# Performance work log

Hardware: AMD Instinct MI355X
Metric: run time of the kernel (lower is better)

Reference implementation:

```python
import jax, jax.numpy as jnp
import numpy as np

B, C, S, N, V = 8, 16, 512, 512, 128
EPS = 1e-5

def setup_inputs() -> dict:
    key = jax.random.key(0)
    ks = jax.random.split(key, 9)
    def u(k, shape, scale):
        return jax.random.uniform(k, shape, jnp.float32, -scale, scale)
    attn_scale = 12 * np.sqrt(3.0 / (S * N * V))      # custom attn_init for query / key.left / value2
    xav_vs = np.sqrt(6.0 / (V + S))                    # xavier_uniform for (C, V, S) or (C, S, V)
    xav_nv = np.sqrt(6.0 / (N + V))                    # xavier_uniform for (C, N, V)
    return {
        "x": jax.random.normal(ks[0], (B, C, S, N), jnp.float32),
        "wq": u(ks[1], (C, N, V), attn_scale),          # query weight (other_features=S)
        "k_left": u(ks[2], (C, V, S), attn_scale),      # key left (attn_init)
        "k_right": u(ks[3], (C, N, V), xav_nv),         # key right (xavier)
        "v1_left": u(ks[4], (C, V, S), xav_vs),         # value1 left (xavier, attn_init=False)
        "v1_right": u(ks[5], (C, N, V), attn_scale),    # value1 right (attn_init scale)
        "v2_w": u(ks[6], (C, V, S), attn_scale),        # value2 weight (other_features=N)
        "gamma": jnp.ones((C,), jnp.float32),
        "beta": jnp.zeros((C,), jnp.float32),
    }

def batch_scaler(y, gamma, beta):
    # normalize over dims (0, 2, 3); per-channel affine
    mean = jnp.mean(y, axis=(0, 2, 3), keepdims=True)
    var = jnp.mean(jnp.square(y - mean), axis=(0, 2, 3), keepdims=True)
    yhat = (y - mean) * jax.lax.rsqrt(var + EPS)
    return yhat * gamma[None, :, None, None] + beta[None, :, None, None]

def reference(x, wq, k_left, k_right, v1_left, v1_right, v2_w, gamma, beta):
    # x: [B,C,S,N]
    q = jnp.matmul(x, wq)                               # [B,C,S,V]
    k = jnp.matmul(jnp.matmul(k_left, x), k_right)       # (C,V,S)@x -> [B,C,V,N] @ (C,N,V) -> [B,C,V,V]
    attn = jax.nn.softmax(jnp.einsum('bcsv,bcwv->bcsw', q, k), axis=-1)  # q @ k^T, softmax last dim
    v1 = jnp.matmul(jnp.matmul(v1_left, x), v1_right)    # [B,C,V,V]
    v2 = jnp.matmul(v2_w, x)                             # [B,C,V,N]
    v = jnp.matmul(v1, v2)                               # [B,C,V,N]
    y = x + jnp.matmul(attn, v)                          # [B,C,S,N]
    return batch_scaler(y, gamma, beta)
```

## Files before the change

### kernel.cpp

```cpp
#include <hip/hip_runtime.h>
#include <math.h>


typedef short  bf16x8 __attribute__((ext_vector_type(8)));
typedef short  short8 __attribute__((ext_vector_type(8)));
typedef float  f32x4  __attribute__((ext_vector_type(4)));

__device__ __forceinline__ unsigned short f2bf(float f) {
    union { float f; unsigned u; } v; v.f = f;
    return (unsigned short)((v.u + 0x7FFF + ((v.u >> 16) & 1)) >> 16);
}
__device__ __forceinline__ float bf2f(unsigned short u) {
    union { unsigned u; float f; } v; v.u = (unsigned)u << 16; return v.f;
}

__device__ __forceinline__ void gload16(const void* g, void* l)
{
    __builtin_amdgcn_global_load_lds(
        (const __attribute__((address_space(1))) void*)g,
        (__attribute__((address_space(3))) void*)l, 16, 0, 0);
}

constexpr size_t OB_XB   = 0;
constexpr size_t OB_XT   = OB_XB  + 67108864;
constexpr size_t OB_KLB  = OB_XT  + 67108864;
constexpr size_t OB_V1LB = OB_KLB + 2097152;
constexpr size_t OB_V2WB = OB_V1LB+ 2097152;
constexpr size_t OB_WQT  = OB_V2WB+ 2097152;
constexpr size_t OB_KRT  = OB_WQT + 2097152;
constexpr size_t OB_V1RT = OB_KRT + 2097152;
constexpr size_t OB_BUF  = OB_V1RT+ 2097152;
constexpr size_t OB_V2T  = OB_BUF + 33554432;
constexpr size_t OB_KM   = OB_V2T + 16777216;
constexpr size_t OB_V1M  = OB_KM  + 4194304;
constexpr size_t OB_ATT  = OB_V1M + 4194304;
constexpr size_t OB_VT   = OB_ATT + 16777216;
constexpr size_t OB_ST   = OB_VT  + 16777216;

template<int NSTEPS, int MF, int NF>
__device__ __forceinline__ void mmcore(const char* __restrict__ Ab, int ldaB,
                                       const char* __restrict__ Bb, int ldbB,
                                       f32x4 (&acc)[MF][NF],
                                       char* __restrict__ smA, char* __restrict__ smB,
                                       int wm, int wn)
{
    const int tid = threadIdx.x;
    const int w = tid >> 6, l = tid & 63, g = l >> 4, lr = l & 15;
    const int rl = l >> 3, ch = l & 7;

#pragma unroll 1
    for (int t = 0; t < NSTEPS; ++t) {
#pragma unroll
        for (int j = 0; j < 4; ++j) {
            const int row = w * 32 + j * 8 + rl;
            gload16(Ab + (size_t)row * ldaB + t * 128 + ((ch ^ (row & 7)) * 16),
                    smA + (w * 32 + j * 8) * 128);
        }
#pragma unroll
        for (int j = 0; j < 4; ++j) {
            const int row = w * 32 + j * 8 + rl;
            gload16(Bb + (size_t)row * ldbB + t * 128 + ((ch ^ (row & 7)) * 16),
                    smB + (w * 32 + j * 8) * 128);
        }
        __syncthreads();
#pragma unroll
        for (int ks = 0; ks < 2; ++ks) {
            bf16x8 av[MF], bv[NF];
            const int cc = ks * 4 + g;
#pragma unroll
            for (int i = 0; i < MF; ++i) { int rw = wm + i * 16 + lr;
                av[i] = *(const bf16x8*)(smA + rw * 128 + ((cc ^ (rw & 7)) * 16)); }
#pragma unroll
            for (int j = 0; j < NF; ++j) { int rw = wn + j * 16 + lr;
                bv[j] = *(const bf16x8*)(smB + rw * 128 + ((cc ^ (rw & 7)) * 16)); }
#pragma unroll
            for (int i = 0; i < MF; ++i)
#pragma unroll
                for (int j = 0; j < NF; ++j)
                    acc[i][j] = __builtin_amdgcn_mfma_f32_16x16x32_bf16(av[i], bv[j], acc[i][j], 0, 0, 0);
        }
        __syncthreads();
    }
}

__device__ __forceinline__ void epi_write_rm(const f32x4 (&acc)[4][4], char* sm)
{
    const int tid = threadIdx.x, w = tid >> 6, l = tid & 63, g = l >> 4, lr = l & 15;
    const int wm = (w >> 1) * 64, wn = (w & 1) * 64;
#pragma unroll
    for (int i = 0; i < 4; ++i)
#pragma unroll
        for (int j = 0; j < 4; ++j) {
            const int row = wm + i * 16 + g * 4, col = wn + j * 16 + lr;
#pragma unroll
            for (int r = 0; r < 4; ++r)
                *(unsigned short*)(sm + (row + r) * 272 + col * 2) = f2bf(acc[i][j][r]);
        }
}

__device__ __forceinline__ void epi_write_tr(const f32x4 (&acc)[4][4], char* sm)
{
    const int tid = threadIdx.x, w = tid >> 6, l = tid & 63, g = l >> 4, lr = l & 15;
    const int wm = (w >> 1) * 64, wn = (w & 1) * 64;
#pragma unroll
    for (int i = 0; i < 4; ++i)
#pragma unroll
        for (int j = 0; j < 4; ++j) {
            const int rv = wm + i * 16 + g * 4, cn = wn + j * 16 + lr;
            ushort4 pk = make_ushort4(f2bf(acc[i][j][0]), f2bf(acc[i][j][1]),
                                      f2bf(acc[i][j][2]), f2bf(acc[i][j][3]));
            *(ushort4*)(sm + cn * 272 + rv * 2) = pk;
        }
}

__device__ __forceinline__ void epi_flush(const char* sm, unsigned short* gout, int ldg)
{
    const int tid = threadIdx.x;
    const int r0 = tid >> 4, q = tid & 15;
#pragma unroll
    for (int rep = 0; rep < 8; ++rep) {
        const int row = rep * 16 + r0;
        *(short8*)((short*)gout + (size_t)row * ldg + q * 8) =
            *(const short8*)(sm + row * 272 + q * 16);
    }
    __syncthreads();
}

__global__ __launch_bounds__(256) void k_prep(const float* __restrict__ kl,
                                              const float* __restrict__ v1l,
                                              const float* __restrict__ v2w,
                                              const float* __restrict__ wq,
                                              const float* __restrict__ kr,
                                              const float* __restrict__ v1r,
                                              unsigned short* __restrict__ klb,
                                              unsigned short* __restrict__ v1lb,
                                              unsigned short* __restrict__ v2wb,
                                              unsigned short* __restrict__ wqt,
                                              unsigned short* __restrict__ krt,
                                              unsigned short* __restrict__ v1rt,
                                              float* __restrict__ stats)
{
    __shared__ float tl[64][65];
    const int id = blockIdx.x, tid = threadIdx.x;
    if (id == 0 && tid < 64) stats[tid] = 0.f;
    if (id < 192) {
        const int sel = id >> 6, blk = id & 63;
        const float* src = sel == 0 ? kl : sel == 1 ? v1l : v2w;
        unsigned short* dst = sel == 0 ? klb : sel == 1 ? v1lb : v2wb;
#pragma unroll
        for (int r = 0; r < 4; ++r) {
            const int i = blk * 1024 + r * 256 + tid;
            float4 v = ((const float4*)src)[i];
            ((ushort4*)dst)[i] = make_ushort4(f2bf(v.x), f2bf(v.y), f2bf(v.z), f2bf(v.w));
        }
        return;
    }
    const int id2 = id - 192;
    const int p = id2 >> 4, rem = id2 & 15, by = rem >> 1, bx = rem & 1;
    const int widx = p >> 4, c = p & 15;
    const float* s = (widx == 0 ? wq : widx == 1 ? kr : v1r) + (size_t)c * 65536;
    unsigned short* d = (widx == 0 ? wqt : widx == 1 ? krt : v1rt) + (size_t)c * 65536;
    const int r0 = by * 64, c0 = bx * 64;
    const int rr = tid >> 4, cc = (tid & 15) * 4;
#pragma unroll
    for (int rep = 0; rep < 4; ++rep) {
        int row = rep * 16 + rr;
        float4 v = *(const float4*)(s + (size_t)(r0 + row) * 128 + c0 + cc);
        tl[cc + 0][row] = v.x; tl[cc + 1][row] = v.y; tl[cc + 2][row] = v.z; tl[cc + 3][row] = v.w;
    }
    __syncthreads();
#pragma unroll
    for (int rep = 0; rep < 4; ++rep) {
        int crow = rep * 16 + rr;
        *(ushort4*)(d + (size_t)(c0 + crow) * 512 + r0 + cc) =
            make_ushort4(f2bf(tl[crow][cc]), f2bf(tl[crow][cc + 1]),
                         f2bf(tl[crow][cc + 2]), f2bf(tl[crow][cc + 3]));
    }
}

__global__ __launch_bounds__(256) void ktransx(const float* __restrict__ x,
                                               unsigned short* __restrict__ xb,
                                               unsigned short* __restrict__ xt)
{
    __shared__ float tl[64][65];
    const int bc = blockIdx.z;
    const int r0 = blockIdx.y * 64, c0 = blockIdx.x * 64;
    const float* src = x + (size_t)bc * 262144;
    const int tid = threadIdx.x, rr = tid >> 4, cc = (tid & 15) * 4;
#pragma unroll
    for (int rep = 0; rep < 4; ++rep) {
        int row = rep * 16 + rr;
        float4 v = *(const float4*)(src + (size_t)(r0 + row) * 512 + c0 + cc);
        *(ushort4*)(xb + (size_t)bc * 262144 + (size_t)(r0 + row) * 512 + c0 + cc) =
            make_ushort4(f2bf(v.x), f2bf(v.y), f2bf(v.z), f2bf(v.w));
        tl[cc + 0][row] = v.x; tl[cc + 1][row] = v.y; tl[cc + 2][row] = v.z; tl[cc + 3][row] = v.w;
    }
    __syncthreads();
#pragma unroll
    for (int rep = 0; rep < 4; ++rep) {
        int crow = rep * 16 + rr;
        *(ushort4*)(xt + (size_t)bc * 262144 + (size_t)(c0 + crow) * 512 + r0 + cc) =
            make_ushort4(f2bf(tl[crow][cc]), f2bf(tl[crow][cc + 1]),
                         f2bf(tl[crow][cc + 2]), f2bf(tl[crow][cc + 3]));
    }
}

__global__ __launch_bounds__(256, 2) void k_wx(const unsigned short* __restrict__ klb,
                                               const unsigned short* __restrict__ v1lb,
                                               const unsigned short* __restrict__ v2wb,
                                               const unsigned short* __restrict__ xt,
                                               unsigned short* __restrict__ bufb,
                                               unsigned short* __restrict__ v2t)
{
    __shared__ char smem[34816];
    char* smA = smem; char* smB = smem + 16384;
    const int mt = blockIdx.x >> 2, n0 = blockIdx.x & 3, bc = blockIdx.y, c = bc & 15;
    const unsigned short* W = mt == 0 ? klb : mt == 1 ? v1lb : v2wb;
    const char* Bb = (const char*)(xt + (size_t)bc * 262144 + (size_t)n0 * 65536);
    const int w = threadIdx.x >> 6;
    f32x4 acc[4][4] = {};
    mmcore<8, 4, 4>((const char*)(W + (size_t)c * 65536), 1024, Bb, 1024, acc, smA, smB,
                    (w >> 1) * 64, (w & 1) * 64);
    if (mt < 2) {
        epi_write_rm(acc, smem);
        __syncthreads();
        epi_flush(smem, bufb + (size_t)bc * 131072 + (size_t)mt * 65536 + n0 * 128, 512);
    } else {
        epi_write_tr(acc, smem);
        __syncthreads();
        epi_flush(smem, v2t + (size_t)bc * 65536 + (size_t)n0 * 16384, 128);
    }
}

__global__ __launch_bounds__(256, 2) void k_kr(const unsigned short* __restrict__ bufb,
                                               const unsigned short* __restrict__ krt,
                                               const unsigned short* __restrict__ v1rt,
                                               unsigned short* __restrict__ kmat,
                                               unsigned short* __restrict__ v1m)
{
    __shared__ char smem[34816];
    char* smA = smem; char* smB = smem + 16384;
    const int mt = blockIdx.x, bc = blockIdx.y, c = bc & 15;
    const int w = threadIdx.x >> 6;
    f32x4 acc[4][4] = {};
    mmcore<8, 4, 4>((const char*)(bufb + (size_t)bc * 131072 + (size_t)mt * 65536), 1024,
                    (const char*)((mt ? v1rt : krt) + (size_t)c * 65536), 1024, acc, smA, smB,
                    (w >> 1) * 64, (w & 1) * 64);
    epi_write_rm(acc, smem);
    __syncthreads();
    epi_flush(smem, (mt ? v1m : kmat) + (size_t)bc * 16384, 128);
}

__global__ __launch_bounds__(256, 2) void k_qat(const unsigned short* __restrict__ xb,
                                                const unsigned short* __restrict__ wqt,
                                                const unsigned short* __restrict__ kmat,
                                                unsigned short* __restrict__ attn)
{
    __shared__ char smem[65536];
    char* smA = smem;
    char* smB = smem + 16384;
    char* qlds = smem + 32768;
    const int mt = blockIdx.x, bc = blockIdx.y, c = bc & 15;
    const int tid = threadIdx.x, w = tid >> 6, l = tid & 63, g = l >> 4, lr = l & 15;

    f32x4 acc[4][4] = {};
    mmcore<8, 4, 4>((const char*)(xb + (size_t)bc * 262144 + (size_t)mt * 65536), 1024,
                    (const char*)(wqt + (size_t)c * 65536), 1024, acc, smA, smB,
                    (w >> 1) * 64, (w & 1) * 64);

    {
        const int wm = (w >> 1) * 64, wn = (w & 1) * 64;
        const int t = wn >> 6;
#pragma unroll
        for (int i = 0; i < 4; ++i)
#pragma unroll
            for (int j = 0; j < 4; ++j) {
                const int k6 = j * 16 + lr;
                const int chunk = k6 >> 3, eb = (k6 & 7) << 1;
#pragma unroll
                for (int r = 0; r < 4; ++r) {
                    const int row = wm + i * 16 + g * 4 + r;
                    *(unsigned short*)(qlds + t * 16384 + row * 128 +
                                       ((chunk ^ (row & 7)) << 4) + eb) = f2bf(acc[i][j][r]);
                }
            }
    }
    __syncthreads();

    f32x4 acc2[2][8] = {};
    const int rl = l >> 3, ch = l & 7;
    const char* Kb = (const char*)(kmat + (size_t)bc * 16384);
#pragma unroll
    for (int t = 0; t < 2; ++t) {
#pragma unroll
        for (int j = 0; j < 4; ++j) {
            const int row = w * 32 + j * 8 + rl;
            gload16(Kb + (size_t)row * 256 + t * 128 + ((ch ^ (row & 7)) * 16),
                    smB + (w * 32 + j * 8) * 128);
        }
        __syncthreads();
#pragma unroll
        for (int ks = 0; ks < 2; ++ks) {
            const int cc2 = ks * 4 + g;
            bf16x8 av[2], bv[8];
#pragma unroll
            for (int i = 0; i < 2; ++i) { const int rw = w * 32 + i * 16 + lr;
                av[i] = *(const bf16x8*)(qlds + t * 16384 + rw * 128 + ((cc2 ^ (rw & 7)) * 16)); }
#pragma unroll
            for (int j = 0; j < 8; ++j) { const int rw = j * 16 + lr;
                bv[j] = *(const bf16x8*)(smB + rw * 128 + ((cc2 ^ (rw & 7)) * 16)); }
#pragma unroll
            for (int i = 0; i < 2; ++i)
#pragma unroll
                for (int j = 0; j < 8; ++j)
                    acc2[i][j] = __builtin_amdgcn_mfma_f32_16x16x32_bf16(av[i], bv[j], acc2[i][j], 0, 0, 0);
        }
        __syncthreads();
    }

    char* wsl = smem + w * 8704;
    unsigned short* ob = attn + (size_t)bc * 65536 + (size_t)(mt * 128 + w * 32) * 128;
#pragma unroll
    for (int i = 0; i < 2; ++i)
#pragma unroll
        for (int r = 0; r < 4; ++r) {
            float mx = -3e38f;
#pragma unroll
            for (int fj = 0; fj < 8; ++fj) mx = fmaxf(mx, acc2[i][fj][r]);
#pragma unroll
            for (int d = 1; d < 16; d <<= 1) mx = fmaxf(mx, __shfl_xor(mx, d));
            float s = 0.f, e[8];
#pragma unroll
            for (int fj = 0; fj < 8; ++fj) { e[fj] = __expf(acc2[i][fj][r] - mx); s += e[fj]; }
#pragma unroll
            for (int d = 1; d < 16; d <<= 1) s += __shfl_xor(s, d);
            const float inv = 1.f / s;
            const int rowh = i * 16 + g * 4 + r;
#pragma unroll
            for (int fj = 0; fj < 8; ++fj)
                *(unsigned short*)(wsl + rowh * 272 + (fj * 16 + lr) * 2) = f2bf(e[fj] * inv);
        }
#pragma unroll
    for (int rep = 0; rep < 8; ++rep) {
        const int row = rep * 4 + (l >> 4);
        *(short8*)((short*)ob + (size_t)row * 128 + (l & 15) * 8) =
            *(const short8*)(wsl + row * 272 + (l & 15) * 16);
    }
}

__global__ __launch_bounds__(256, 2) void k_v(const unsigned short* __restrict__ v2t,
                                              const unsigned short* __restrict__ v1m,
                                              unsigned short* __restrict__ vt)
{
    __shared__ char smem[34816];
    char* smA = smem; char* smB = smem + 16384;
    const int mt = blockIdx.x, bc = blockIdx.y;
    const int w = threadIdx.x >> 6;
    f32x4 acc[4][4] = {};
    mmcore<2, 4, 4>((const char*)(v2t + (size_t)bc * 65536 + (size_t)mt * 16384), 256,
                    (const char*)(v1m + (size_t)bc * 16384), 256, acc, smA, smB,
                    (w >> 1) * 64, (w & 1) * 64);
    epi_write_rm(acc, smem);
    __syncthreads();
    epi_flush(smem, vt + (size_t)bc * 65536 + (size_t)mt * 16384, 128);
}

__global__ __launch_bounds__(256, 2) void k_y(const unsigned short* __restrict__ attn,
                                              const unsigned short* __restrict__ vt,
                                              const float* __restrict__ x,
                                              unsigned short* __restrict__ yb,
                                              float* __restrict__ stats)
{
    __shared__ char smem[34816];
    __shared__ float r1[4], r2[4];
    char* smA = smem; char* smB = smem + 16384;
    const int nx = blockIdx.x, my = blockIdx.y, bc = blockIdx.z, c = bc & 15;
    const int tid = threadIdx.x, w = tid >> 6, l = tid & 63, g = l >> 4, lr = l & 15;
    f32x4 acc[4][4] = {};
    mmcore<2, 4, 4>((const char*)(attn + (size_t)bc * 65536 + (size_t)my * 16384), 256,
                    (const char*)(vt + (size_t)bc * 65536 + (size_t)nx * 16384), 256, acc, smA, smB,
                    (w >> 1) * 64, (w & 1) * 64);
    const float* xw = x + (size_t)bc * 262144 + (size_t)my * 128 * 512 + nx * 128;
    const int wm = (w >> 1) * 64, wn = (w & 1) * 64;
    float lsum = 0.f, lss = 0.f;
#pragma unroll
    for (int i = 0; i < 4; ++i)
#pragma unroll
        for (int j = 0; j < 4; ++j)
#pragma unroll
            for (int r = 0; r < 4; ++r) {
                const int row = wm + i * 16 + g * 4 + r, col = wn + j * 16 + lr;
                const float yv = acc[i][j][r] + xw[(size_t)row * 512 + col];
                lsum += yv; lss += yv * yv;
                *(unsigned short*)(smem + row * 272 + col * 2) = f2bf(yv);
            }
#pragma unroll
    for (int d = 32; d >= 1; d >>= 1) { lsum += __shfl_xor(lsum, d); lss += __shfl_xor(lss, d); }
    if (l == 0) { r1[w] = lsum; r2[w] = lss; }
    __syncthreads();
    epi_flush(smem, yb + (size_t)bc * 262144 + (size_t)my * 128 * 512 + nx * 128, 512);
    if (tid == 0) {
        atomicAdd(&stats[c * 2 + 0], r1[0] + r1[1] + r1[2] + r1[3]);
        atomicAdd(&stats[c * 2 + 1], r2[0] + r2[1] + r2[2] + r2[3]);
    }
}

__global__ __launch_bounds__(256) void k_norm(const unsigned short* __restrict__ yb,
                                              float* __restrict__ out,
                                              const float* __restrict__ stats,
                                              const float* __restrict__ gamma,
                                              const float* __restrict__ beta)
{
    __shared__ float ssc[16], ssh[16];
    if (threadIdx.x < 16) {
        const int c = threadIdx.x;
        const float cnt  = 2097152.f;
        const float mean = stats[c * 2 + 0] / cnt;
        const float var  = stats[c * 2 + 1] / cnt - mean * mean;
        const float sc   = rsqrtf(var + 1e-5f) * gamma[c];
        ssc[c] = sc;
        ssh[c] = beta[c] - mean * sc;
    }
    __syncthreads();
    const int tot = 4194304;
    for (int i = blockIdx.x * 256 + threadIdx.x; i < tot; i += gridDim.x * 256) {
        const long e = (long)i * 8;
        const int c = (int)(e >> 18) & 15;
        const float sc = ssc[c];
        const float sh = ssh[c];
        short8 v = ((const short8*)yb)[i];
        float4 o0, o1;
        o0.x = bf2f((unsigned short)v[0]) * sc + sh;
        o0.y = bf2f((unsigned short)v[1]) * sc + sh;
        o0.z = bf2f((unsigned short)v[2]) * sc + sh;
        o0.w = bf2f((unsigned short)v[3]) * sc + sh;
        o1.x = bf2f((unsigned short)v[4]) * sc + sh;
        o1.y = bf2f((unsigned short)v[5]) * sc + sh;
        o1.z = bf2f((unsigned short)v[6]) * sc + sh;
        o1.w = bf2f((unsigned short)v[7]) * sc + sh;
        ((float4*)out)[(size_t)i * 2 + 0] = o0;
        ((float4*)out)[(size_t)i * 2 + 1] = o1;
    }
}

extern "C" void kernel_launch(void* const* d_in, const int* in_sizes, int n_in,
                              void* d_out, int out_size, void* d_ws, size_t ws_size,
                              hipStream_t stream)
{
    (void)in_sizes; (void)n_in; (void)out_size; (void)ws_size;
    const float* x     = (const float*)d_in[0];
    const float* wq    = (const float*)d_in[1];
    const float* kl    = (const float*)d_in[2];
    const float* kr    = (const float*)d_in[3];
    const float* v1l   = (const float*)d_in[4];
    const float* v1r   = (const float*)d_in[5];
    const float* v2w   = (const float*)d_in[6];
    const float* gamma = (const float*)d_in[7];
    const float* beta  = (const float*)d_in[8];
    float* out = (float*)d_out;
    char*  ws  = (char*)d_ws;

    unsigned short* xb   = (unsigned short*)(ws + OB_XB);
    unsigned short* yb   = xb;
    unsigned short* xt   = (unsigned short*)(ws + OB_XT);
    unsigned short* klb  = (unsigned short*)(ws + OB_KLB);
    unsigned short* v1lb = (unsigned short*)(ws + OB_V1LB);
    unsigned short* v2wb = (unsigned short*)(ws + OB_V2WB);
    unsigned short* wqt  = (unsigned short*)(ws + OB_WQT);
    unsigned short* krt  = (unsigned short*)(ws + OB_KRT);
    unsigned short* v1rt = (unsigned short*)(ws + OB_V1RT);
    unsigned short* bufb = (unsigned short*)(ws + OB_BUF);
    unsigned short* v2t  = (unsigned short*)(ws + OB_V2T);
    unsigned short* kmat = (unsigned short*)(ws + OB_KM);
    unsigned short* v1m  = (unsigned short*)(ws + OB_V1M);
    unsigned short* attn = (unsigned short*)(ws + OB_ATT);
    unsigned short* vt   = (unsigned short*)(ws + OB_VT);
    float*          st   = (float*)(ws + OB_ST);

    hipLaunchKernelGGL(k_prep,  dim3(960),       dim3(256), 0, stream,
                       kl, v1l, v2w, wq, kr, v1r, klb, v1lb, v2wb, wqt, krt, v1rt, st);
    hipLaunchKernelGGL(ktransx, dim3(8, 8, 128), dim3(256), 0, stream, x, xb, xt);
    hipLaunchKernelGGL(k_wx,    dim3(12, 128),   dim3(256), 0, stream, klb, v1lb, v2wb, xt, bufb, v2t);
    hipLaunchKernelGGL(k_kr,    dim3(2, 128),    dim3(256), 0, stream, bufb, krt, v1rt, kmat, v1m);
    hipLaunchKernelGGL(k_qat,   dim3(4, 128),    dim3(256), 0, stream, xb, wqt, kmat, attn);
    hipLaunchKernelGGL(k_v,     dim3(4, 128),    dim3(256), 0, stream, v2t, v1m, vt);
    hipLaunchKernelGGL(k_y,     dim3(4, 4, 128), dim3(256), 0, stream, attn, vt, x, yb, st);
    hipLaunchKernelGGL(k_norm,  dim3(2048),      dim3(256), 0, stream, yb, out, st, gamma, beta);
}
```

Baseline: 241.8 us.

## Fuse attention softmax with attn@V and merge weight-times-x GEMMs per block

Merges the query/attention/softmax kernel with the attn@V residual kernel. The softmaxed attention tile stays in LDS and is reused across all four N column tiles, so the bf16 attention matrix no longer goes through global memory and one launch is removed. k_wx also now computes all three weight GEMMs in one block instead of spreading them across separate blocks, which cuts its grid to a third. The trade-offs are less parallelism in both kernels, longer serial work per block, and y stores that write 2-byte values straight to global memory instead of being staged through LDS.

```diff
diff --git a/kernel.cpp b/kernel.cpp
--- a/kernel.cpp
+++ b/kernel.cpp
@@ -33,8 +33,7 @@
 constexpr size_t OB_V2T  = OB_BUF + 33554432;
 constexpr size_t OB_KM   = OB_V2T + 16777216;
 constexpr size_t OB_V1M  = OB_KM  + 4194304;
-constexpr size_t OB_ATT  = OB_V1M + 4194304;
-constexpr size_t OB_VT   = OB_ATT + 16777216;
+constexpr size_t OB_VT   = OB_V1M + 4194304;
 constexpr size_t OB_ST   = OB_VT  + 16777216;
 
 template<int NSTEPS, int MF, int NF>
@@ -214,18 +213,27 @@
 {
     __shared__ char smem[34816];
     char* smA = smem; char* smB = smem + 16384;
-    const int mt = blockIdx.x >> 2, n0 = blockIdx.x & 3, bc = blockIdx.y, c = bc & 15;
-    const unsigned short* W = mt == 0 ? klb : mt == 1 ? v1lb : v2wb;
+    const int n0 = blockIdx.x, bc = blockIdx.y, c = bc & 15;
     const char* Bb = (const char*)(xt + (size_t)bc * 262144 + (size_t)n0 * 65536);
     const int w = threadIdx.x >> 6;
-    f32x4 acc[4][4] = {};
-    mmcore<8, 4, 4>((const char*)(W + (size_t)c * 65536), 1024, Bb, 1024, acc, smA, smB,
-                    (w >> 1) * 64, (w & 1) * 64);
-    if (mt < 2) {
+    const int wm = (w >> 1) * 64, wn = (w & 1) * 64;
+    {
+        f32x4 acc[4][4] = {};
+        mmcore<8, 4, 4>((const char*)(klb + (size_t)c * 65536), 1024, Bb, 1024, acc, smA, smB, wm, wn);
         epi_write_rm(acc, smem);
         __syncthreads();
-        epi_flush(smem, bufb + (size_t)bc * 131072 + (size_t)mt * 65536 + n0 * 128, 512);
-    } else {
+        epi_flush(smem, bufb + (size_t)bc * 131072 + n0 * 128, 512);
+    }
+    {
+        f32x4 acc[4][4] = {};
+        mmcore<8, 4, 4>((const char*)(v1lb + (size_t)c * 65536), 1024, Bb, 1024, acc, smA, smB, wm, wn);
+        epi_write_rm(acc, smem);
+        __syncthreads();
+        epi_flush(smem, bufb + (size_t)bc * 131072 + 65536 + n0 * 128, 512);
+    }
+    {
+        f32x4 acc[4][4] = {};
+        mmcore<8, 4, 4>((const char*)(v2wb + (size_t)c * 65536), 1024, Bb, 1024, acc, smA, smB, wm, wn);
         epi_write_tr(acc, smem);
         __syncthreads();
         epi_flush(smem, v2t + (size_t)bc * 65536 + (size_t)n0 * 16384, 128);
@@ -251,103 +259,6 @@
     epi_flush(smem, (mt ? v1m : kmat) + (size_t)bc * 16384, 128);
 }
 
-__global__ __launch_bounds__(256, 2) void k_qat(const unsigned short* __restrict__ xb,
-                                                const unsigned short* __restrict__ wqt,
-                                                const unsigned short* __restrict__ kmat,
-                                                unsigned short* __restrict__ attn)
-{
-    __shared__ char smem[65536];
-    char* smA = smem;
-    char* smB = smem + 16384;
-    char* qlds = smem + 32768;
-    const int mt = blockIdx.x, bc = blockIdx.y, c = bc & 15;
-    const int tid = threadIdx.x, w = tid >> 6, l = tid & 63, g = l >> 4, lr = l & 15;
-
-    f32x4 acc[4][4] = {};
-    mmcore<8, 4, 4>((const char*)(xb + (size_t)bc * 262144 + (size_t)mt * 65536), 1024,
-                    (const char*)(wqt + (size_t)c * 65536), 1024, acc, smA, smB,
-                    (w >> 1) * 64, (w & 1) * 64);
-
-    {
-        const int wm = (w >> 1) * 64, wn = (w & 1) * 64;
-        const int t = wn >> 6;
-#pragma unroll
-        for (int i = 0; i < 4; ++i)
-#pragma unroll
-            for (int j = 0; j < 4; ++j) {
-                const int k6 = j * 16 + lr;
-                const int chunk = k6 >> 3, eb = (k6 & 7) << 1;
-#pragma unroll
-                for (int r = 0; r < 4; ++r) {
-                    const int row = wm + i * 16 + g * 4 + r;
-                    *(unsigned short*)(qlds + t * 16384 + row * 128 +
-                                       ((chunk ^ (row & 7)) << 4) + eb) = f2bf(acc[i][j][r]);
-                }
-            }
-    }
-    __syncthreads();
-
-    f32x4 acc2[2][8] = {};
-    const int rl = l >> 3, ch = l & 7;
-    const char* Kb = (const char*)(kmat + (size_t)bc * 16384);
-#pragma unroll
-    for (int t = 0; t < 2; ++t) {
-#pragma unroll
-        for (int j = 0; j < 4; ++j) {
-            const int row = w * 32 + j * 8 + rl;
-            gload16(Kb + (size_t)row * 256 + t * 128 + ((ch ^ (row & 7)) * 16),
-                    smB + (w * 32 + j * 8) * 128);
-        }
-        __syncthreads();
-#pragma unroll
-        for (int ks = 0; ks < 2; ++ks) {
-            const int cc2 = ks * 4 + g;
-            bf16x8 av[2], bv[8];
-#pragma unroll
-            for (int i = 0; i < 2; ++i) { const int rw = w * 32 + i * 16 + lr;
-                av[i] = *(const bf16x8*)(qlds + t * 16384 + rw * 128 + ((cc2 ^ (rw & 7)) * 16)); }
-#pragma unroll
-            for (int j = 0; j < 8; ++j) { const int rw = j * 16 + lr;
-                bv[j] = *(const bf16x8*)(smB + rw * 128 + ((cc2 ^ (rw & 7)) * 16)); }
-#pragma unroll
-            for (int i = 0; i < 2; ++i)
-#pragma unroll
-                for (int j = 0; j < 8; ++j)
-                    acc2[i][j] = __builtin_amdgcn_mfma_f32_16x16x32_bf16(av[i], bv[j], acc2[i][j], 0, 0, 0);
-        }
-        __syncthreads();
-    }
-
-    char* wsl = smem + w * 8704;
-    unsigned short* ob = attn + (size_t)bc * 65536 + (size_t)(mt * 128 + w * 32) * 128;
-#pragma unroll
-    for (int i = 0; i < 2; ++i)
-#pragma unroll
-        for (int r = 0; r < 4; ++r) {
-            float mx = -3e38f;
-#pragma unroll
-            for (int fj = 0; fj < 8; ++fj) mx = fmaxf(mx, acc2[i][fj][r]);
-#pragma unroll
-            for (int d = 1; d < 16; d <<= 1) mx = fmaxf(mx, __shfl_xor(mx, d));
-            float s = 0.f, e[8];
-#pragma unroll
-            for (int fj = 0; fj < 8; ++fj) { e[fj] = __expf(acc2[i][fj][r] - mx); s += e[fj]; }
-#pragma unroll
-            for (int d = 1; d < 16; d <<= 1) s += __shfl_xor(s, d);
-            const float inv = 1.f / s;
-            const int rowh = i * 16 + g * 4 + r;
-#pragma unroll
-            for (int fj = 0; fj < 8; ++fj)
-                *(unsigned short*)(wsl + rowh * 272 + (fj * 16 + lr) * 2) = f2bf(e[fj] * inv);
-        }
-#pragma unroll
-    for (int rep = 0; rep < 8; ++rep) {
-        const int row = rep * 4 + (l >> 4);
-        *(short8*)((short*)ob + (size_t)row * 128 + (l & 15) * 8) =
-            *(const short8*)(wsl + row * 272 + (l & 15) * 16);
-    }
-}
-
 __global__ __launch_bounds__(256, 2) void k_v(const unsigned short* __restrict__ v2t,
                                               const unsigned short* __restrict__ v1m,
                                               unsigned short* __restrict__ vt)
@@ -365,40 +276,156 @@
     epi_flush(smem, vt + (size_t)bc * 65536 + (size_t)mt * 16384, 128);
 }
 
-__global__ __launch_bounds__(256, 2) void k_y(const unsigned short* __restrict__ attn,
-                                              const unsigned short* __restrict__ vt,
-                                              const float* __restrict__ x,
-                                              unsigned short* __restrict__ yb,
-                                              float* __restrict__ stats)
-{
-    __shared__ char smem[34816];
+__global__ __launch_bounds__(256, 2) void k_qaty(const unsigned short* __restrict__ xb,
+                                                 const unsigned short* __restrict__ wqt,
+                                                 const unsigned short* __restrict__ kmat,
+                                                 const unsigned short* __restrict__ vt,
+                                                 const float* __restrict__ x,
+                                                 unsigned short* __restrict__ yb,
+                                                 float* __restrict__ stats)
+{
+    __shared__ char smem[65536];
     __shared__ float r1[4], r2[4];
-    char* smA = smem; char* smB = smem + 16384;
-    const int nx = blockIdx.x, my = blockIdx.y, bc = blockIdx.z, c = bc & 15;
+    char* smA = smem;
+    char* smB = smem + 16384;
+    char* qlds = smem + 32768;
+    const int mt = blockIdx.x, bc = blockIdx.y, c = bc & 15;
     const int tid = threadIdx.x, w = tid >> 6, l = tid & 63, g = l >> 4, lr = l & 15;
-    f32x4 acc[4][4] = {};
-    mmcore<2, 4, 4>((const char*)(attn + (size_t)bc * 65536 + (size_t)my * 16384), 256,
-                    (const char*)(vt + (size_t)bc * 65536 + (size_t)nx * 16384), 256, acc, smA, smB,
-                    (w >> 1) * 64, (w & 1) * 64);
-    const float* xw = x + (size_t)bc * 262144 + (size_t)my * 128 * 512 + nx * 128;
+    const int rl = l >> 3, ch = l & 7;
+
+    {
+        f32x4 acc[4][4] = {};
+        mmcore<8, 4, 4>((const char*)(xb + (size_t)bc * 262144 + (size_t)mt * 65536), 1024,
+                        (const char*)(wqt + (size_t)c * 65536), 1024, acc, smA, smB,
+                        (w >> 1) * 64, (w & 1) * 64);
+        const int wm = (w >> 1) * 64, wn = (w & 1) * 64;
+        const int t = wn >> 6;
+#pragma unroll
+        for (int i = 0; i < 4; ++i)
+#pragma unroll
+            for (int j = 0; j < 4; ++j) {
+                const int k6 = j * 16 + lr;
+                const int chunk = k6 >> 3, eb = (k6 & 7) << 1;
+#pragma unroll
+                for (int r = 0; r < 4; ++r) {
+                    const int row = wm + i * 16 + g * 4 + r;
+                    *(unsigned short*)(qlds + t * 16384 + row * 128 +
+                                       ((chunk ^ (row & 7)) << 4) + eb) = f2bf(acc[i][j][r]);
+                }
+            }
+    }
+    __syncthreads();
+
+    f32x4 acc2[2][8] = {};
+    {
+        const char* Kb = (const char*)(kmat + (size_t)bc * 16384);
+#pragma unroll
+        for (int t = 0; t < 2; ++t) {
+#pragma unroll
+            for (int j = 0; j < 4; ++j) {
+                const int row = w * 32 + j * 8 + rl;
+                gload16(Kb + (size_t)row * 256 + t * 128 + ((ch ^ (row & 7)) * 16),
+                        smB + (w * 32 + j * 8) * 128);
+            }
+            __syncthreads();
+#pragma unroll
+            for (int ks = 0; ks < 2; ++ks) {
+                const int cc2 = ks * 4 + g;
+                bf16x8 av[2], bv[8];
+#pragma unroll
+                for (int i = 0; i < 2; ++i) { const int rw = w * 32 + i * 16 + lr;
+                    av[i] = *(const bf16x8*)(qlds + t * 16384 + rw * 128 + ((cc2 ^ (rw & 7)) * 16)); }
+#pragma unroll
+                for (int j = 0; j < 8; ++j) { const int rw = j * 16 + lr;
+                    bv[j] = *(const bf16x8*)(smB + rw * 128 + ((cc2 ^ (rw & 7)) * 16)); }
+#pragma unroll
+                for (int i = 0; i < 2; ++i)
+#pragma unroll
+                    for (int j = 0; j < 8; ++j)
+                        acc2[i][j] = __builtin_amdgcn_mfma_f32_16x16x32_bf16(av[i], bv[j], acc2[i][j], 0, 0, 0);
+            }
+            __syncthreads();
+        }
+    }
+
+#pragma unroll
+    for (int i = 0; i < 2; ++i)
+#pragma unroll
+        for (int r = 0; r < 4; ++r) {
+            float mx = -3e38f;
+#pragma unroll
+            for (int fj = 0; fj < 8; ++fj) mx = fmaxf(mx, acc2[i][fj][r]);
+#pragma unroll
+            for (int d = 1; d < 16; d <<= 1) mx = fmaxf(mx, __shfl_xor(mx, d));
+            float s = 0.f, e[8];
+#pragma unroll
+            for (int fj = 0; fj < 8; ++fj) { e[fj] = __expf(acc2[i][fj][r] - mx); s += e[fj]; }
+#pragma unroll
+            for (int d = 1; d < 16; d <<= 1) s += __shfl_xor(s, d);
+            const float inv = 1.f / s;
+            const int row = w * 32 + i * 16 + g * 4 + r;
+#pragma unroll
+            for (int fj = 0; fj < 8; ++fj) {
+                const int col = fj * 16 + lr;
+                const int t = fj >> 2, k6 = col & 63;
+                const int chunk = k6 >> 3, eb = (k6 & 7) << 1;
+                *(unsigned short*)(qlds + t * 16384 + row * 128 +
+                                   ((chunk ^ (row & 7)) << 4) + eb) = f2bf(e[fj] * inv);
+            }
+        }
+    __syncthreads();
+
+    float lsum = 0.f, lss = 0.f;
     const int wm = (w >> 1) * 64, wn = (w & 1) * 64;
-    float lsum = 0.f, lss = 0.f;
-#pragma unroll
-    for (int i = 0; i < 4; ++i)
-#pragma unroll
-        for (int j = 0; j < 4; ++j)
-#pragma unroll
-            for (int r = 0; r < 4; ++r) {
-                const int row = wm + i * 16 + g * 4 + r, col = wn + j * 16 + lr;
-                const float yv = acc[i][j][r] + xw[(size_t)row * 512 + col];
-                lsum += yv; lss += yv * yv;
-                *(unsigned short*)(smem + row * 272 + col * 2) = f2bf(yv);
+#pragma unroll 1
+    for (int nx = 0; nx < 4; ++nx) {
+        f32x4 acc3[4][4] = {};
+        const char* Vb = (const char*)(vt + (size_t)bc * 65536 + (size_t)nx * 16384);
+#pragma unroll
+        for (int t = 0; t < 2; ++t) {
+#pragma unroll
+            for (int j = 0; j < 4; ++j) {
+                const int row = w * 32 + j * 8 + rl;
+                gload16(Vb + (size_t)row * 256 + t * 128 + ((ch ^ (row & 7)) * 16),
+                        smB + (w * 32 + j * 8) * 128);
             }
+            __syncthreads();
+#pragma unroll
+            for (int ks = 0; ks < 2; ++ks) {
+                const int cc2 = ks * 4 + g;
+                bf16x8 av[4], bv[4];
+#pragma unroll
+                for (int i = 0; i < 4; ++i) { const int rw = wm + i * 16 + lr;
+                    av[i] = *(const bf16x8*)(qlds + t * 16384 + rw * 128 + ((cc2 ^ (rw & 7)) * 16)); }
+#pragma unroll
+                for (int j = 0; j < 4; ++j) { const int rw = wn + j * 16 + lr;
+                    bv[j] = *(const bf16x8*)(smB + rw * 128 + ((cc2 ^ (rw & 7)) * 16)); }
+#pragma unroll
+                for (int i = 0; i < 4; ++i)
+#pragma unroll
+                    for (int j = 0; j < 4; ++j)
+                        acc3[i][j] = __builtin_amdgcn_mfma_f32_16x16x32_bf16(av[i], bv[j], acc3[i][j], 0, 0, 0);
+            }
+            __syncthreads();
+        }
+        const float* xw = x + (size_t)bc * 262144 + (size_t)(mt * 128) * 512 + nx * 128;
+        unsigned short* yw = yb + (size_t)bc * 262144 + (size_t)(mt * 128) * 512 + nx * 128;
+#pragma unroll
+        for (int i = 0; i < 4; ++i)
+#pragma unroll
+            for (int j = 0; j < 4; ++j)
+#pragma unroll
+                for (int r = 0; r < 4; ++r) {
+                    const int row = wm + i * 16 + g * 4 + r, col = wn + j * 16 + lr;
+                    const float yv = acc3[i][j][r] + xw[(size_t)row * 512 + col];
+                    lsum += yv; lss += yv * yv;
+                    yw[(size_t)row * 512 + col] = f2bf(yv);
+                }
+    }
 #pragma unroll
     for (int d = 32; d >= 1; d >>= 1) { lsum += __shfl_xor(lsum, d); lss += __shfl_xor(lss, d); }
     if (l == 0) { r1[w] = lsum; r2[w] = lss; }
     __syncthreads();
-    epi_flush(smem, yb + (size_t)bc * 262144 + (size_t)my * 128 * 512 + nx * 128, 512);
     if (tid == 0) {
         atomicAdd(&stats[c * 2 + 0], r1[0] + r1[1] + r1[2] + r1[3]);
         atomicAdd(&stats[c * 2 + 1], r2[0] + r2[1] + r2[2] + r2[3]);
@@ -473,17 +500,15 @@
     unsigned short* v2t  = (unsigned short*)(ws + OB_V2T);
     unsigned short* kmat = (unsigned short*)(ws + OB_KM);
     unsigned short* v1m  = (unsigned short*)(ws + OB_V1M);
-    unsigned short* attn = (unsigned short*)(ws + OB_ATT);
     unsigned short* vt   = (unsigned short*)(ws + OB_VT);
     float*          st   = (float*)(ws + OB_ST);
 
     hipLaunchKernelGGL(k_prep,  dim3(960),       dim3(256), 0, stream,
                        kl, v1l, v2w, wq, kr, v1r, klb, v1lb, v2wb, wqt, krt, v1rt, st);
     hipLaunchKernelGGL(ktransx, dim3(8, 8, 128), dim3(256), 0, stream, x, xb, xt);
-    hipLaunchKernelGGL(k_wx,    dim3(12, 128),   dim3(256), 0, stream, klb, v1lb, v2wb, xt, bufb, v2t);
+    hipLaunchKernelGGL(k_wx,    dim3(4, 128),    dim3(256), 0, stream, klb, v1lb, v2wb, xt, bufb, v2t);
     hipLaunchKernelGGL(k_kr,    dim3(2, 128),    dim3(256), 0, stream, bufb, krt, v1rt, kmat, v1m);
-    hipLaunchKernelGGL(k_qat,   dim3(4, 128),    dim3(256), 0, stream, xb, wqt, kmat, attn);
     hipLaunchKernelGGL(k_v,     dim3(4, 128),    dim3(256), 0, stream, v2t, v1m, vt);
-    hipLaunchKernelGGL(k_y,     dim3(4, 4, 128), dim3(256), 0, stream, attn, vt, x, yb, st);
+    hipLaunchKernelGGL(k_qaty,  dim3(4, 128),    dim3(256), 0, stream, xb, wqt, kmat, vt, x, yb, st);
     hipLaunchKernelGGL(k_norm,  dim3(2048),      dim3(256), 0, stream, yb, out, st, gamma, beta);
 }
```

Measured after the change: 325.7 us. +34.7%, slower.
